# Kernel optimization log

Measured on AMD Instinct MI355X. Metric: run time of the kernel, lower is better.

## Reference

```python
import jax, jax.numpy as jnp
import numpy as np

NUM_BLOCKS = 8
LAMBDA = 0.01  # sparsity_threshold


def _softshrink(x, lam):
    return jnp.sign(x) * jnp.maximum(jnp.abs(x) - lam, 0.0)


def _groups(T):
    # Group timesteps t by their padded FFT length P = max(8, 1 << (t+1).bit_length()).
    gs = {}
    for t in range(T):
        P = max(8, 1 << (t + 1).bit_length())
        gs.setdefault(P, []).append(t)
    return [(P, np.asarray(ts, dtype=np.int32)) for P, ts in sorted(gs.items())]


def setup_inputs() -> dict:
    key = jax.random.key(0)
    k1, k2, k3, k4, k5 = jax.random.split(key, 5)
    B, T, C = 4, 256, 256
    nb = NUM_BLOCKS
    bs = C // nb
    scale = 0.02
    return {
        "x": jax.random.normal(k1, (B, T, C), dtype=jnp.float32),
        "w1": scale * jax.random.normal(k2, (2, nb, bs, bs), dtype=jnp.float32),
        "b1": scale * jax.random.normal(k3, (2, nb, bs), dtype=jnp.float32),
        "w2": scale * jax.random.normal(k4, (2, nb, bs, bs), dtype=jnp.float32),
        "b2": scale * jax.random.normal(k5, (2, nb, bs), dtype=jnp.float32),
    }


def reference(x, w1, b1, w2, b2):
    B, T, C = x.shape
    nb = NUM_BLOCKS
    bs = C // nb
    out = jnp.zeros_like(x)
    for P, ts in _groups(T):  # O(log T) static groups
        G = len(ts)
        L = min(P, T)
        ts_j = jnp.asarray(ts)
        # x padded/truncated to FFT length P
        xp = jnp.zeros((B, P, C), dtype=x.dtype).at[:, :L, :].set(x[:, :L, :])
        # causal mask per timestep in group: keep positions j <= t
        mask = jnp.arange(P)[None, :] <= ts_j[:, None]  # (G, P)
        xg = jnp.where(mask[:, None, :, None], xp[None], 0.0)  # (G,B,P,C)
        xf = jnp.fft.fft(xg, axis=2, norm="ortho").reshape(G, B, P, nb, bs)
        re, im = xf.real, xf.imag
        o1r = jax.nn.relu(jnp.einsum("gbtni,nio->gbtno", re, w1[0])
                          - jnp.einsum("gbtni,nio->gbtno", im, w1[1]) + b1[0])
        o1i = jax.nn.relu(jnp.einsum("gbtni,nio->gbtno", im, w1[0])
                          + jnp.einsum("gbtni,nio->gbtno", re, w1[1]) + b1[1])
        o2r = (jnp.einsum("gbtno,noi->gbtni", o1r, w2[0])
               - jnp.einsum("gbtno,noi->gbtni", o1i, w2[1]) + b2[0])
        o2i = (jnp.einsum("gbtno,noi->gbtni", o1i, w2[0])
               + jnp.einsum("gbtno,noi->gbtni", o1r, w2[1]) + b2[1])
        o2r = _softshrink(o2r, LAMBDA)
        o2i = _softshrink(o2i, LAMBDA)
        xc = (o2r + 1j * o2i).reshape(G, B, P, C)
        xi = jnp.fft.ifft(xc, axis=2, norm="ortho").real  # (G,B,P,C)
        vals = xi[jnp.arange(G), :, ts_j, :]  # (G,B,C): row t of each per-t iFFT
        out = out.at[:, ts_j, :].set(jnp.transpose(vals, (1, 0, 2)))
    return out + x
```

## Files before the change

kernel.cpp:

```cpp
#include <hip/hip_runtime.h>
#include <math.h>

#define LAM 0.01f

typedef __bf16 bf16x8 __attribute__((ext_vector_type(8)));
typedef float f32x4 __attribute__((ext_vector_type(4)));
typedef short short8v __attribute__((ext_vector_type(8)));
typedef short short4v __attribute__((ext_vector_type(4)));

#define BF(v) __builtin_bit_cast(bf16x8, (v))
#define MFMA __builtin_amdgcn_mfma_f32_16x16x32_bf16
#define XROW 36
#define LDS_FENCE() do { asm volatile("s_waitcnt lgkmcnt(0)" ::: "memory"); \
                         __builtin_amdgcn_sched_barrier(0); } while (0)

__device__ __forceinline__ unsigned short f2bf(float f) {
    __bf16 h = (__bf16)f;
    return __builtin_bit_cast(unsigned short, h);
}
__device__ __forceinline__ float bf2f(unsigned short u) {
    unsigned int v = ((unsigned int)u) << 16;
    return __builtin_bit_cast(float, v);
}

struct Task { int sh, c16, t_lo, t_hi, jump_s; };
__device__ __forceinline__ Task task_params(int tau) {
    Task tk;
    if (tau < 16)       { tk.sh = 0; tk.c16 = tau * 2; tk.t_lo = 255; tk.t_hi = 255; tk.jump_s = 256; }
    else if (tau < 144) { int u = tau - 16;  int seg = u >> 4; tk.sh = 1; tk.c16 = u & 15;
                          tk.t_lo = 127 + 16 * seg; tk.t_hi = tk.t_lo + 15; tk.jump_s = tk.t_lo + 1; }
    else if (tau < 176) { int u = tau - 144; int seg = u >> 3; tk.sh = 2; tk.c16 = u & 7;
                          tk.t_lo = 63 + 16 * seg; tk.t_hi = tk.t_lo + 15; tk.jump_s = tk.t_lo + 1; }
    else if (tau < 184) { int u = tau - 176; int seg = u >> 2; tk.sh = 3; tk.c16 = u & 3;
                          tk.t_lo = 31 + 16 * seg; tk.t_hi = tk.t_lo + 15; tk.jump_s = tk.t_lo + 1; }
    else if (tau < 186) { tk.sh = 4; tk.c16 = tau - 184; tk.t_lo = 15; tk.t_hi = 30; tk.jump_s = 0; }
    else if (tau == 186){ tk.sh = 5; tk.c16 = 0; tk.t_lo = 7; tk.t_hi = 14; tk.jump_s = 0; }
    else                { tk.sh = 6; tk.c16 = 0; tk.t_lo = 0; tk.t_hi = 6;  tk.jump_s = 0; }
    return tk;
}

__global__ __launch_bounds__(256, 3)
void afno_mfma(const float* __restrict__ x,
               const float* __restrict__ w1,
               const float* __restrict__ b1,
               const float* __restrict__ w2,
               const float* __restrict__ b2,
               float* __restrict__ out) {
    __shared__ unsigned short xs[256 * XROW];
    __shared__ float twc[544];
    __shared__ float tws[544];
    __shared__ float jslab[4 * 544];

    int bid = blockIdx.x;
    int w  = bid >> 5;
    int bn = bid & 31;
    int b = bn >> 3, n = bn & 7;

    int tid = threadIdx.x;
    int wv = tid >> 6;
    int lane = tid & 63;
    int lg = lane >> 4;
    int l15 = lane & 15;
    int krow = lg * 8;

    int rows = 0;
    #pragma unroll
    for (int q = 0; q < 4; ++q) {
        Task t2 = task_params((w << 2) | q);
        rows = rows > (t2.t_hi + 1) ? rows : (t2.t_hi + 1);
    }
    rows = (rows + 31) & ~31;
    rows = rows > 256 ? 256 : rows;
    for (int idx = tid; idx < rows * 16; idx += 256) {
        int row = idx >> 4, cp = idx & 15;
        float2 v = *(const float2*)(x + (b * 256 + row) * 256 + n * 32 + cp * 2);
        unsigned int pk = (unsigned int)f2bf(v.x) | ((unsigned int)f2bf(v.y) << 16);
        *(unsigned int*)(xs + row * XROW + cp * 2) = pk;
    }
    for (int m = tid; m < 512; m += 256) {
        float sv, cv;
        sincosf(6.28318530717958647692f * (float)m * (1.0f / 512.0f), &sv, &cv);
        twc[m + (m >> 4)] = cv;
        tws[m + (m >> 4)] = sv;
    }

    Task tk = task_params((w << 2) | wv);
    int P = 512 >> tk.sh;
    float invSqrtP = rsqrtf((float)P);

    const float* w1r = w1 + n * 1024;
    const float* w1i = w1 + (8 + n) * 1024;
    const float* w2r = w2 + n * 1024;
    const float* w2i = w2 + (8 + n) * 1024;
    short8v W10[2], W11[2], W11n[2], W20[2], W21[2], W21n[2];
    #pragma unroll
    for (int h = 0; h < 2; ++h) {
        int col = h * 16 + l15;
        #pragma unroll
        for (int j = 0; j < 8; ++j) {
            W10[h][j]  = (short)f2bf(w1r[(krow + j) * 32 + col] * invSqrtP);
            W11[h][j]  = (short)f2bf(w1i[(krow + j) * 32 + col] * invSqrtP);
            W11n[h][j] = W11[h][j] ^ (short)0x8000;
            int crow = ((j >> 2) * 16) + (lg * 4) + (j & 3);
            W20[h][j]  = (short)f2bf(w2r[crow * 32 + col]);
            W21[h][j]  = (short)f2bf(w2i[crow * 32 + col]);
            W21n[h][j] = W21[h][j] ^ (short)0x8000;
        }
    }
    f32x4 b1rv[2], b1iv[2];
    float b2r_[2], b2i_[2];
    #pragma unroll
    for (int h = 0; h < 2; ++h) {
        int base = n * 32 + h * 16 + lg * 4;
        b1rv[h] = f32x4{b1[base], b1[base + 1], b1[base + 2], b1[base + 3]};
        b1iv[h] = f32x4{b1[256 + base], b1[256 + base + 1], b1[256 + base + 2], b1[256 + base + 3]};
        b2r_[h] = b2[n * 32 + h * 16 + l15];
        b2i_[h] = b2[256 + n * 32 + h * 16 + l15];
    }
    __syncthreads();

    int pA5 = 0, mA5 = 0;
    int prow5[4], mrow5[4];
    float Xre[8] = {0,0,0,0,0,0,0,0}, Xim[8] = {0,0,0,0,0,0,0,0};

#define JUMP_X(js_) do { \
        f32x4 jre0 = {0,0,0,0}, jre1 = {0,0,0,0}, jim0 = {0,0,0,0}, jim1 = {0,0,0,0}; \
        int nkk_ = ((js_) + 31) >> 5; \
        int tail_ = (js_) & 31; \
        for (int kk = 0; kk < nkk_; ++kk) { \
            int sb_ = kk * 32; \
            short8v ac_, an2_; \
            bool zb_ = (tail_ != 0) && (kk == nkk_ - 1) && (krow >= tail_); \
            if (zb_) { \
                _Pragma("unroll") \
                for (int j = 0; j < 8; ++j) { ac_[j] = 0; an2_[j] = 0; } \
            } else { \
                int mj_ = (pA5 * (sb_ + krow)) & 511; \
                _Pragma("unroll") \
                for (int j = 0; j < 8; ++j) { \
                    int mi2_ = mj_ + (mj_ >> 4); \
                    ac_[j]  = (short)f2bf(twc[mi2_]); \
                    an2_[j] = (short)f2bf(-tws[mi2_]); \
                    mj_ = (mj_ + pA5) & 511; \
                } \
            } \
            short8v bx0_, bx1_; \
            _Pragma("unroll") \
            for (int j = 0; j < 8; ++j) { \
                int base_ = (sb_ + krow + j) * XROW + l15; \
                bx0_[j] = (short)xs[base_]; \
                bx1_[j] = (short)xs[base_ + 16]; \
            } \
            jre0 = MFMA(BF(ac_),  BF(bx0_), jre0, 0, 0, 0); \
            jim0 = MFMA(BF(an2_), BF(bx0_), jim0, 0, 0, 0); \
            jre1 = MFMA(BF(ac_),  BF(bx1_), jre1, 0, 0, 0); \
            jim1 = MFMA(BF(an2_), BF(bx1_), jim1, 0, 0, 0); \
        } \
        float* jt_ = jslab + wv * 544; \
        _Pragma("unroll") \
        for (int r = 0; r < 4; ++r) { \
            jt_[(lg * 4 + r) * 33 + l15]      = jre0[r]; \
            jt_[(lg * 4 + r) * 33 + 16 + l15] = jre1[r]; \
        } \
        LDS_FENCE(); \
        _Pragma("unroll") \
        for (int j = 0; j < 8; ++j) Xre[j] = jt_[l15 * 33 + krow + j]; \
        LDS_FENCE(); \
        _Pragma("unroll") \
        for (int r = 0; r < 4; ++r) { \
            jt_[(lg * 4 + r) * 33 + l15]      = jim0[r]; \
            jt_[(lg * 4 + r) * 33 + 16 + l15] = jim1[r]; \
        } \
        LDS_FENCE(); \
        _Pragma("unroll") \
        for (int j = 0; j < 8; ++j) Xim[j] = jt_[l15 * 33 + krow + j]; \
        LDS_FENCE(); \
    } while (0)

#define UPDATE_X(sidx) do { \
        int mi_ = mA5 + (mA5 >> 4); \
        float tc_ = twc[mi_], tsn_ = tws[mi_]; \
        mA5 = (mA5 + pA5) & 511; \
        short4v xa_ = *(const short4v*)(xs + (sidx) * XROW + krow); \
        short4v xb_ = *(const short4v*)(xs + (sidx) * XROW + krow + 4); \
        _Pragma("unroll") \
        for (int j = 0; j < 4; ++j) { \
            float xf = bf2f((unsigned short)xa_[j]); \
            Xre[j] = fmaf(xf, tc_, Xre[j]); \
            Xim[j] = fmaf(xf, -tsn_, Xim[j]); \
            float xg = bf2f((unsigned short)xb_[j]); \
            Xre[4 + j] = fmaf(xg, tc_, Xre[4 + j]); \
            Xim[4 + j] = fmaf(xg, -tsn_, Xim[4 + j]); \
        } } while (0)

#define STEP_CORE(sidx, do_upd, DEST) do { \
        if (do_upd) UPDATE_X(sidx); \
        short8v ar_, ai_; \
        _Pragma("unroll") \
        for (int j = 0; j < 8; ++j) { \
            ar_[j] = (short)f2bf(Xre[j]); \
            ai_[j] = (short)f2bf(Xim[j]); \
        } \
        f32x4 o1r_[2], o1i_[2]; \
        _Pragma("unroll") \
        for (int h = 0; h < 2; ++h) { \
            o1r_[h] = MFMA(BF(W10[h]),  BF(ar_), b1rv[h], 0, 0, 0); \
            o1r_[h] = MFMA(BF(W11n[h]), BF(ai_), o1r_[h], 0, 0, 0); \
            o1i_[h] = MFMA(BF(W10[h]),  BF(ai_), b1iv[h], 0, 0, 0); \
            o1i_[h] = MFMA(BF(W11[h]),  BF(ar_), o1i_[h], 0, 0, 0); \
        } \
         \
        short8v a2r_, a2i_; \
        _Pragma("unroll") \
        for (int j = 0; j < 8; ++j) { \
            a2r_[j] = (short)f2bf(fmaxf(o1r_[j >> 2][j & 3], 0.f)); \
            a2i_[j] = (short)f2bf(fmaxf(o1i_[j >> 2][j & 3], 0.f)); \
        } \
        f32x4 o2r_[2], o2i_[2]; \
        _Pragma("unroll") \
        for (int h = 0; h < 2; ++h) { \
            f32x4 cr = {b2r_[h], b2r_[h], b2r_[h], b2r_[h]}; \
            f32x4 ci = {b2i_[h], b2i_[h], b2i_[h], b2i_[h]}; \
            o2r_[h] = MFMA(BF(a2r_), BF(W20[h]), cr, 0, 0, 0); \
            o2r_[h] = MFMA(BF(a2i_), BF(W21n[h]), o2r_[h], 0, 0, 0); \
            o2i_[h] = MFMA(BF(a2i_), BF(W20[h]), ci, 0, 0, 0); \
            o2i_[h] = MFMA(BF(a2r_), BF(W21[h]), o2i_[h], 0, 0, 0); \
        } \
        float sh0 = 0.f, sh1 = 0.f; \
        _Pragma("unroll") \
        for (int r = 0; r < 4; ++r) { \
            int mi_ = mrow5[r] + (mrow5[r] >> 4); \
            float tc_ = twc[mi_], tsn_ = tws[mi_]; \
            mrow5[r] = (mrow5[r] + prow5[r]) & 511; \
            float v0r = o2r_[0][r]; v0r -= __builtin_amdgcn_fmed3f(v0r, -LAM, LAM); \
            float v0i = o2i_[0][r]; v0i -= __builtin_amdgcn_fmed3f(v0i, -LAM, LAM); \
            sh0 = fmaf(v0r, tc_, sh0); sh0 = fmaf(-v0i, tsn_, sh0); \
            float v1r = o2r_[1][r]; v1r -= __builtin_amdgcn_fmed3f(v1r, -LAM, LAM); \
            float v1i = o2i_[1][r]; v1i -= __builtin_amdgcn_fmed3f(v1i, -LAM, LAM); \
            sh1 = fmaf(v1r, tc_, sh1); sh1 = fmaf(-v1i, tsn_, sh1); \
        } \
        sh0 += __shfl_xor(sh0, 16); \
        sh1 += __shfl_xor(sh1, 16); \
        if (P > 8) { sh0 += __shfl_xor(sh0, 32); sh1 += __shfl_xor(sh1, 32); } \
        DEST = (lane & 16) ? sh1 : sh0; \
    } while (0)

    if (tk.jump_s == 256) {
        float acc = 0.f;
        for (int nc = 0; nc < 2; ++nc) {
            int cb_ = (tk.c16 + nc) * 16;
            pA5 = (cb_ + l15) & 511;
            #pragma unroll
            for (int r = 0; r < 4; ++r) {
                prow5[r] = (cb_ + lg * 4 + r) & 511;
                mrow5[r] = (prow5[r] * 255) & 511;
            }
            JUMP_X(256);
            float v_;
            STEP_CORE(255, false, v_);
            acc += v_;
        }
        if (lane < 32)
            atomicAdd(out + (b * 256 + 255) * 256 + n * 32 + (lane & 31), acc * invSqrtP);
        return;
    }

    int cbase = tk.c16 * 16;
    pA5 = ((cbase + l15) << tk.sh) & 511;
    #pragma unroll
    for (int r = 0; r < 4; ++r) {
        prow5[r] = ((cbase + lg * 4 + r) << tk.sh) & 511;
        mrow5[r] = (prow5[r] * tk.t_lo) & 511;
    }

    bool jumped = tk.jump_s > 0;
    if (jumped) {
        JUMP_X(tk.jump_s);
        mA5 = (pA5 * tk.jump_s) & 511;
    } else {
        for (int s = 0; s < tk.t_lo; ++s) UPDATE_X(s);
    }

    int s = tk.t_lo;
    bool skip0 = jumped;
    while (s + 1 <= tk.t_hi) {
        {
            float v_;
            STEP_CORE(s, !skip0, v_);
            if (lane < 32)
                atomicAdd(out + (b * 256 + s) * 256 + n * 32 + (lane & 31), v_ * invSqrtP);
        }
        {
            float v_;
            STEP_CORE(s + 1, true, v_);
            if (lane < 32)
                atomicAdd(out + (b * 256 + s + 1) * 256 + n * 32 + (lane & 31), v_ * invSqrtP);
        }
        skip0 = false;
        s += 2;
    }
    if (s <= tk.t_hi) {
        float v_;
        STEP_CORE(s, !skip0, v_);
        if (lane < 32)
            atomicAdd(out + (b * 256 + s) * 256 + n * 32 + (lane & 31), v_ * invSqrtP);
    }
}

extern "C" void kernel_launch(void* const* d_in, const int* in_sizes, int n_in,
                              void* d_out, int out_size, void* d_ws, size_t ws_size,
                              hipStream_t stream) {
    const float* x  = (const float*)d_in[0];
    const float* w1 = (const float*)d_in[1];
    const float* b1 = (const float*)d_in[2];
    const float* w2 = (const float*)d_in[3];
    const float* b2 = (const float*)d_in[4];
    float* out = (float*)d_out;

    hipMemcpyAsync(out, x, (size_t)(4 * 256 * 256) * sizeof(float),
                   hipMemcpyDeviceToDevice, stream);
    hipLaunchKernelGGL(afno_mfma, dim3(1504), dim3(256), 0, stream,
                       x, w1, b1, w2, b2, out);
}
```

Measured before the change: 58.20 us.

## Interleave two timesteps per step and pack twiddles into float2

Each loop iteration now computes two consecutive timesteps with interleaved MFMA chains, which exposes more independent work and hides MFMA latency. Cosine and sine twiddles are stored together as float2 so one LDS load fetches both. The jump prefix now stops at t_lo so every step uses a uniform update, and the tail zeroing becomes a per-element predicate. The cost is higher register pressure from keeping two timesteps live, which could lower occupancy.

New measurement: 56.52 us. -2.9%, faster.

```diff
diff --git a/kernel.cpp b/kernel.cpp
--- a/kernel.cpp
+++ b/kernel.cpp
@@ -28,11 +28,11 @@
     Task tk;
     if (tau < 16)       { tk.sh = 0; tk.c16 = tau * 2; tk.t_lo = 255; tk.t_hi = 255; tk.jump_s = 256; }
     else if (tau < 144) { int u = tau - 16;  int seg = u >> 4; tk.sh = 1; tk.c16 = u & 15;
-                          tk.t_lo = 127 + 16 * seg; tk.t_hi = tk.t_lo + 15; tk.jump_s = tk.t_lo + 1; }
+                          tk.t_lo = 127 + 16 * seg; tk.t_hi = tk.t_lo + 15; tk.jump_s = tk.t_lo; }
     else if (tau < 176) { int u = tau - 144; int seg = u >> 3; tk.sh = 2; tk.c16 = u & 7;
-                          tk.t_lo = 63 + 16 * seg; tk.t_hi = tk.t_lo + 15; tk.jump_s = tk.t_lo + 1; }
+                          tk.t_lo = 63 + 16 * seg; tk.t_hi = tk.t_lo + 15; tk.jump_s = tk.t_lo; }
     else if (tau < 184) { int u = tau - 176; int seg = u >> 2; tk.sh = 3; tk.c16 = u & 3;
-                          tk.t_lo = 31 + 16 * seg; tk.t_hi = tk.t_lo + 15; tk.jump_s = tk.t_lo + 1; }
+                          tk.t_lo = 31 + 16 * seg; tk.t_hi = tk.t_lo + 15; tk.jump_s = tk.t_lo; }
     else if (tau < 186) { tk.sh = 4; tk.c16 = tau - 184; tk.t_lo = 15; tk.t_hi = 30; tk.jump_s = 0; }
     else if (tau == 186){ tk.sh = 5; tk.c16 = 0; tk.t_lo = 7; tk.t_hi = 14; tk.jump_s = 0; }
     else                { tk.sh = 6; tk.c16 = 0; tk.t_lo = 0; tk.t_hi = 6;  tk.jump_s = 0; }
@@ -47,8 +47,7 @@
                const float* __restrict__ b2,
                float* __restrict__ out) {
     __shared__ unsigned short xs[256 * XROW];
-    __shared__ float twc[544];
-    __shared__ float tws[544];
+    __shared__ float2 tw[544];
     __shared__ float jslab[4 * 544];
 
     int bid = blockIdx.x;
@@ -80,8 +79,7 @@
     for (int m = tid; m < 512; m += 256) {
         float sv, cv;
         sincosf(6.28318530717958647692f * (float)m * (1.0f / 512.0f), &sv, &cv);
-        twc[m + (m >> 4)] = cv;
-        tws[m + (m >> 4)] = sv;
+        tw[m + (m >> 4)] = make_float2(cv, sv);
     }
 
     Task tk = task_params((w << 2) | wv);
@@ -126,23 +124,18 @@
 #define JUMP_X(js_) do { \
         f32x4 jre0 = {0,0,0,0}, jre1 = {0,0,0,0}, jim0 = {0,0,0,0}, jim1 = {0,0,0,0}; \
         int nkk_ = ((js_) + 31) >> 5; \
-        int tail_ = (js_) & 31; \
         for (int kk = 0; kk < nkk_; ++kk) { \
             int sb_ = kk * 32; \
             short8v ac_, an2_; \
-            bool zb_ = (tail_ != 0) && (kk == nkk_ - 1) && (krow >= tail_); \
-            if (zb_) { \
-                _Pragma("unroll") \
-                for (int j = 0; j < 8; ++j) { ac_[j] = 0; an2_[j] = 0; } \
-            } else { \
-                int mj_ = (pA5 * (sb_ + krow)) & 511; \
-                _Pragma("unroll") \
-                for (int j = 0; j < 8; ++j) { \
-                    int mi2_ = mj_ + (mj_ >> 4); \
-                    ac_[j]  = (short)f2bf(twc[mi2_]); \
-                    an2_[j] = (short)f2bf(-tws[mi2_]); \
-                    mj_ = (mj_ + pA5) & 511; \
-                } \
+            int mj_ = (pA5 * (sb_ + krow)) & 511; \
+            _Pragma("unroll") \
+            for (int j = 0; j < 8; ++j) { \
+                int mi2_ = mj_ + (mj_ >> 4); \
+                float2 t_ = tw[mi2_]; \
+                bool ok_ = (sb_ + krow + j) < (js_); \
+                ac_[j]  = ok_ ? (short)f2bf(t_.x)  : (short)0; \
+                an2_[j] = ok_ ? (short)f2bf(-t_.y) : (short)0; \
+                mj_ = (mj_ + pA5) & 511; \
             } \
             short8v bx0_, bx1_; \
             _Pragma("unroll") \
@@ -179,70 +172,121 @@
 
 #define UPDATE_X(sidx) do { \
         int mi_ = mA5 + (mA5 >> 4); \
-        float tc_ = twc[mi_], tsn_ = tws[mi_]; \
+        float2 t_ = tw[mi_]; \
         mA5 = (mA5 + pA5) & 511; \
         short4v xa_ = *(const short4v*)(xs + (sidx) * XROW + krow); \
         short4v xb_ = *(const short4v*)(xs + (sidx) * XROW + krow + 4); \
         _Pragma("unroll") \
         for (int j = 0; j < 4; ++j) { \
             float xf = bf2f((unsigned short)xa_[j]); \
-            Xre[j] = fmaf(xf, tc_, Xre[j]); \
-            Xim[j] = fmaf(xf, -tsn_, Xim[j]); \
+            Xre[j] = fmaf(xf, t_.x, Xre[j]); \
+            Xim[j] = fmaf(xf, -t_.y, Xim[j]); \
             float xg = bf2f((unsigned short)xb_[j]); \
-            Xre[4 + j] = fmaf(xg, tc_, Xre[4 + j]); \
-            Xim[4 + j] = fmaf(xg, -tsn_, Xim[4 + j]); \
-        } } while (0)
-
-#define STEP_CORE(sidx, do_upd, DEST) do { \
-        if (do_upd) UPDATE_X(sidx); \
-        short8v ar_, ai_; \
+            Xre[4 + j] = fmaf(xg, t_.x, Xre[4 + j]); \
+            Xim[4 + j] = fmaf(xg, -t_.y, Xim[4 + j]); \
+        } } while (0)
+
+#define SNAP_A(arv, aiv) do { \
         _Pragma("unroll") \
         for (int j = 0; j < 8; ++j) { \
-            ar_[j] = (short)f2bf(Xre[j]); \
-            ai_[j] = (short)f2bf(Xim[j]); \
-        } \
-        f32x4 o1r_[2], o1i_[2]; \
+            (arv)[j] = (short)f2bf(Xre[j]); \
+            (aiv)[j] = (short)f2bf(Xim[j]); \
+        } } while (0)
+
+#define L1(arv, aiv, o1r_, o1i_) do { \
         _Pragma("unroll") \
         for (int h = 0; h < 2; ++h) { \
-            o1r_[h] = MFMA(BF(W10[h]),  BF(ar_), b1rv[h], 0, 0, 0); \
-            o1r_[h] = MFMA(BF(W11n[h]), BF(ai_), o1r_[h], 0, 0, 0); \
-            o1i_[h] = MFMA(BF(W10[h]),  BF(ai_), b1iv[h], 0, 0, 0); \
-            o1i_[h] = MFMA(BF(W11[h]),  BF(ar_), o1i_[h], 0, 0, 0); \
-        } \
-         \
-        short8v a2r_, a2i_; \
+            o1r_[h] = MFMA(BF(arv), BF(W10[h]),  b1rv[h], 0, 0, 0); \
+            o1r_[h] = MFMA(BF(aiv), BF(W11n[h]), o1r_[h], 0, 0, 0); \
+            o1i_[h] = MFMA(BF(aiv), BF(W10[h]),  b1iv[h], 0, 0, 0); \
+            o1i_[h] = MFMA(BF(arv), BF(W11[h]),  o1i_[h], 0, 0, 0); \
+        } } while (0)
+
+#define REPACK(o1r_, o1i_, a2r_, a2i_) do { \
         _Pragma("unroll") \
         for (int j = 0; j < 8; ++j) { \
-            a2r_[j] = (short)f2bf(fmaxf(o1r_[j >> 2][j & 3], 0.f)); \
-            a2i_[j] = (short)f2bf(fmaxf(o1i_[j >> 2][j & 3], 0.f)); \
-        } \
-        f32x4 o2r_[2], o2i_[2]; \
+            (a2r_)[j] = (short)f2bf(fmaxf(o1r_[j >> 2][j & 3], 0.f)); \
+            (a2i_)[j] = (short)f2bf(fmaxf(o1i_[j >> 2][j & 3], 0.f)); \
+        } } while (0)
+
+#define L2(a2r_, a2i_, o2r_, o2i_) do { \
         _Pragma("unroll") \
         for (int h = 0; h < 2; ++h) { \
             f32x4 cr = {b2r_[h], b2r_[h], b2r_[h], b2r_[h]}; \
             f32x4 ci = {b2i_[h], b2i_[h], b2i_[h], b2i_[h]}; \
-            o2r_[h] = MFMA(BF(a2r_), BF(W20[h]), cr, 0, 0, 0); \
+            o2r_[h] = MFMA(BF(a2r_), BF(W20[h]),  cr, 0, 0, 0); \
             o2r_[h] = MFMA(BF(a2i_), BF(W21n[h]), o2r_[h], 0, 0, 0); \
-            o2i_[h] = MFMA(BF(a2i_), BF(W20[h]), ci, 0, 0, 0); \
-            o2i_[h] = MFMA(BF(a2r_), BF(W21[h]), o2i_[h], 0, 0, 0); \
-        } \
+            o2i_[h] = MFMA(BF(a2i_), BF(W20[h]),  ci, 0, 0, 0); \
+            o2i_[h] = MFMA(BF(a2r_), BF(W21[h]),  o2i_[h], 0, 0, 0); \
+        } } while (0)
+
+#define EPI(o2r_, o2i_, tR, DEST) do { \
         float sh0 = 0.f, sh1 = 0.f; \
         _Pragma("unroll") \
         for (int r = 0; r < 4; ++r) { \
-            int mi_ = mrow5[r] + (mrow5[r] >> 4); \
-            float tc_ = twc[mi_], tsn_ = tws[mi_]; \
-            mrow5[r] = (mrow5[r] + prow5[r]) & 511; \
             float v0r = o2r_[0][r]; v0r -= __builtin_amdgcn_fmed3f(v0r, -LAM, LAM); \
             float v0i = o2i_[0][r]; v0i -= __builtin_amdgcn_fmed3f(v0i, -LAM, LAM); \
-            sh0 = fmaf(v0r, tc_, sh0); sh0 = fmaf(-v0i, tsn_, sh0); \
+            sh0 = fmaf(v0r, (tR)[r].x, sh0); sh0 = fmaf(-v0i, (tR)[r].y, sh0); \
             float v1r = o2r_[1][r]; v1r -= __builtin_amdgcn_fmed3f(v1r, -LAM, LAM); \
             float v1i = o2i_[1][r]; v1i -= __builtin_amdgcn_fmed3f(v1i, -LAM, LAM); \
-            sh1 = fmaf(v1r, tc_, sh1); sh1 = fmaf(-v1i, tsn_, sh1); \
+            sh1 = fmaf(v1r, (tR)[r].x, sh1); sh1 = fmaf(-v1i, (tR)[r].y, sh1); \
         } \
         sh0 += __shfl_xor(sh0, 16); \
         sh1 += __shfl_xor(sh1, 16); \
         if (P > 8) { sh0 += __shfl_xor(sh0, 32); sh1 += __shfl_xor(sh1, 32); } \
         DEST = (lane & 16) ? sh1 : sh0; \
+    } while (0)
+
+#define STEP1(sidx, do_upd) do { \
+        if (do_upd) UPDATE_X(sidx); \
+        short8v ar_, ai_, a2r_, a2i_; \
+        SNAP_A(ar_, ai_); \
+        f32x4 o1r_[2], o1i_[2], o2r_[2], o2i_[2]; \
+        L1(ar_, ai_, o1r_, o1i_); \
+        REPACK(o1r_, o1i_, a2r_, a2i_); \
+        L2(a2r_, a2i_, o2r_, o2i_); \
+        float2 tR[4]; \
+        _Pragma("unroll") \
+        for (int r = 0; r < 4; ++r) { \
+            int mi_ = mrow5[r] + (mrow5[r] >> 4); \
+            tR[r] = tw[mi_]; \
+            mrow5[r] = (mrow5[r] + prow5[r]) & 511; \
+        } \
+        float v_; \
+        EPI(o2r_, o2i_, tR, v_); \
+        if (lane < 32) \
+            atomicAdd(out + (b * 256 + (sidx)) * 256 + n * 32 + (lane & 31), v_ * invSqrtP); \
+    } while (0)
+
+#define STEP2(s0) do { \
+        short8v ar0_, ai0_, ar1_, ai1_, a2r0_, a2i0_, a2r1_, a2i1_; \
+        UPDATE_X(s0);     SNAP_A(ar0_, ai0_); \
+        UPDATE_X((s0)+1); SNAP_A(ar1_, ai1_); \
+        f32x4 o1r0_[2], o1i0_[2], o1r1_[2], o1i1_[2]; \
+        L1(ar0_, ai0_, o1r0_, o1i0_); \
+        L1(ar1_, ai1_, o1r1_, o1i1_); \
+        REPACK(o1r0_, o1i0_, a2r0_, a2i0_); \
+        REPACK(o1r1_, o1i1_, a2r1_, a2i1_); \
+        f32x4 o2r0_[2], o2i0_[2], o2r1_[2], o2i1_[2]; \
+        L2(a2r0_, a2i0_, o2r0_, o2i0_); \
+        L2(a2r1_, a2i1_, o2r1_, o2i1_); \
+        float2 tR0[4], tR1[4]; \
+        _Pragma("unroll") \
+        for (int r = 0; r < 4; ++r) { \
+            int m0_ = mrow5[r]; \
+            int m1_ = (m0_ + prow5[r]) & 511; \
+            tR0[r] = tw[m0_ + (m0_ >> 4)]; \
+            tR1[r] = tw[m1_ + (m1_ >> 4)]; \
+            mrow5[r] = (m1_ + prow5[r]) & 511; \
+        } \
+        float v0_, v1_; \
+        EPI(o2r0_, o2i0_, tR0, v0_); \
+        EPI(o2r1_, o2i1_, tR1, v1_); \
+        if (lane < 32) { \
+            float* o_ = out + (b * 256 + (s0)) * 256 + n * 32 + (lane & 31); \
+            atomicAdd(o_, v0_ * invSqrtP); \
+            atomicAdd(o_ + 256, v1_ * invSqrtP); \
+        } \
     } while (0)
 
     if (tk.jump_s == 256) {
@@ -257,7 +301,21 @@
             }
             JUMP_X(256);
             float v_;
-            STEP_CORE(255, false, v_);
+            {
+                short8v ar_, ai_, a2r_, a2i_;
+                SNAP_A(ar_, ai_);
+                f32x4 o1r_[2], o1i_[2], o2r_[2], o2i_[2];
+                L1(ar_, ai_, o1r_, o1i_);
+                REPACK(o1r_, o1i_, a2r_, a2i_);
+                L2(a2r_, a2i_, o2r_, o2i_);
+                float2 tR[4];
+                #pragma unroll
+                for (int r = 0; r < 4; ++r) {
+                    int mi_ = mrow5[r] + (mrow5[r] >> 4);
+                    tR[r] = tw[mi_];
+                }
+                EPI(o2r_, o2i_, tR, v_);
+            }
             acc += v_;
         }
         if (lane < 32)
@@ -273,8 +331,7 @@
         mrow5[r] = (prow5[r] * tk.t_lo) & 511;
     }
 
-    bool jumped = tk.jump_s > 0;
-    if (jumped) {
+    if (tk.jump_s > 0) {
         JUMP_X(tk.jump_s);
         mA5 = (pA5 * tk.jump_s) & 511;
     } else {
@@ -282,28 +339,12 @@
     }
 
     int s = tk.t_lo;
-    bool skip0 = jumped;
     while (s + 1 <= tk.t_hi) {
-        {
-            float v_;
-            STEP_CORE(s, !skip0, v_);
-            if (lane < 32)
-                atomicAdd(out + (b * 256 + s) * 256 + n * 32 + (lane & 31), v_ * invSqrtP);
-        }
-        {
-            float v_;
-            STEP_CORE(s + 1, true, v_);
-            if (lane < 32)
-                atomicAdd(out + (b * 256 + s + 1) * 256 + n * 32 + (lane & 31), v_ * invSqrtP);
-        }
-        skip0 = false;
+        STEP2(s);
         s += 2;
     }
     if (s <= tk.t_hi) {
-        float v_;
-        STEP_CORE(s, !skip0, v_);
-        if (lane < 32)
-            atomicAdd(out + (b * 256 + s) * 256 + n * 32 + (lane & 31), v_ * invSqrtP);
+        STEP1(s, true);
     }
 }
 
```
